# Performance work log

Measured on AMD Instinct MI355X. Metric: run time of the kernel, lower is better.

Reference implementation:

```python
import jax, jax.numpy as jnp
import numpy as np

N = 8192          # total neurons (n)
IN_NEURONS = 1024 # input_neurons
OUT_NEURONS = 256 # output_neurons


def setup_inputs() -> dict:
    key = jax.random.key(0)
    k1, k2 = jax.random.split(key)
    x = jax.random.normal(k1, (1, IN_NEURONS), dtype=jnp.float32)
    # learned adjacency weight (original uses kaiming_uniform; scale kept small for stability)
    W = jax.random.normal(k2, (N, N), dtype=jnp.float32) * 0.01
    return {"x": x, "W": W, "num_steps": 4}


def reference(x, W, num_steps):
    n = W.shape[0]
    # load_input_neurons: state = (W.T * pad(x[0], n)).T  ==  W * s0[:, None]
    s0 = jnp.pad(x[0], (0, n - x.shape[1]))        # [n]
    state = W * s0[:, None]                        # [n, n]

    # step(): next = sum_i(W.T * state[i]) then .T  ==  W * colsum(state)[:, None]
    def body(state, _):
        col_sum = state.sum(axis=0)                # [n]
        return W * col_sum[:, None], None

    state, _ = jax.lax.scan(body, state, None, length=num_steps)

    # extract_output_neurons: diagonal entries state[-i, -i], i = OUT..1
    return jnp.diagonal(state)[-OUT_NEURONS:]      # [OUT_NEURONS]
```

## Files before the change

kernel.cpp:

```cpp
#include <hip/hip_runtime.h>


namespace {
constexpr int N = 8192;
constexpr int NF4 = N / 4;
constexpr int IN_N = 1024;
constexpr int OUT_N = 256;
constexpr int BT = 256;

constexpr int B1 = 256;
constexpr int R1R = IN_N / B1;
constexpr int B2 = 1024;
constexpr int R2R = N / B2;

constexpr size_t OFF_V1 = 0;
constexpr size_t OFF_V2 = 8192;
constexpr size_t OFF_V3 = 16384;
constexpr size_t OFF_V4 = 24576;
constexpr size_t OFF_P  = 32768;

typedef float f4 __attribute__((ext_vector_type(4)));
}

__global__ void zero_vecs(float* __restrict__ ws) {
  int i = blockIdx.x * blockDim.x + threadIdx.x;
  if (i < 3 * N + OUT_N) ws[i] = 0.0f;
}

template <int ROWS>
__global__ __launch_bounds__(BT) void gemv_slab(const float* __restrict__ W,
                                                const float* __restrict__ vin,
                                                float* __restrict__ P) {
  __shared__ float sv[ROWS];
  const int b = blockIdx.x, t = threadIdx.x;
  const int i0 = b * ROWS;
  if (t < ROWS) sv[t] = vin[i0 + t];
  __syncthreads();
  const f4* __restrict__ W4 = reinterpret_cast<const f4*>(W);
  f4 acc[8];
#pragma unroll
  for (int k = 0; k < 8; ++k) acc[k] = (f4)(0.f);
#pragma unroll 2
  for (int i = 0; i < ROWS; ++i) {
    const float s = sv[i];
    const f4* __restrict__ row = W4 + (size_t)(i0 + i) * NF4;
#pragma unroll
    for (int k = 0; k < 8; ++k) {
      const f4 w = __builtin_nontemporal_load(row + k * BT + t);
      acc[k] += w * s;
    }
  }
  f4* __restrict__ P4 = reinterpret_cast<f4*>(P) + (size_t)b * NF4;
#pragma unroll
  for (int k = 0; k < 8; ++k) P4[k * BT + t] = acc[k];
}

template <int CS>
__global__ __launch_bounds__(BT) void reduce_cols(const float* __restrict__ P,
                                                  float* __restrict__ v) {
  const int j = blockIdx.x * BT + threadIdx.x;
  const int c0 = blockIdx.y * CS;
  float a = 0.f;
#pragma unroll 8
  for (int c = 0; c < CS; ++c) a += P[(size_t)(c0 + c) * N + j];
  atomicAdd(v + j, a);
}

__global__ __launch_bounds__(64) void gemv_tail(const float* __restrict__ W,
                                                const float* __restrict__ v3,
                                                float* __restrict__ v4) {
  __shared__ float sv[32];
  const int b = blockIdx.x, t = threadIdx.x;
  const int i0 = b * 32;
  if (t < 32) sv[t] = v3[i0 + t];
  __syncthreads();
  const f4* __restrict__ W4 = reinterpret_cast<const f4*>(W);
  f4 a = (f4)(0.f);
#pragma unroll 4
  for (int i = 0; i < 32; ++i) {
    const f4 w = W4[(size_t)(i0 + i) * NF4 + 1984 + t];
    a += w * sv[i];
  }
  atomicAdd(v4 + 4 * t + 0, a.x);
  atomicAdd(v4 + 4 * t + 1, a.y);
  atomicAdd(v4 + 4 * t + 2, a.z);
  atomicAdd(v4 + 4 * t + 3, a.w);
}

__global__ void diag_scale(const float* __restrict__ W,
                           const float* __restrict__ v4,
                           float* __restrict__ out) {
  const int t = threadIdx.x;
  const size_t j = (size_t)(N - OUT_N + t);
  out[t] = W[j * (N + 1)] * v4[t];
}

extern "C" void kernel_launch(void* const* d_in, const int* in_sizes, int n_in,
                              void* d_out, int out_size, void* d_ws, size_t ws_size,
                              hipStream_t stream) {
  const float* x = (const float*)d_in[0];
  const float* W = (const float*)d_in[1];
  float* ws = (float*)d_ws;
  float* v1 = ws + OFF_V1;
  float* v2 = ws + OFF_V2;
  float* v3 = ws + OFF_V3;
  float* v4 = ws + OFF_V4;
  float* P  = ws + OFF_P;
  float* out = (float*)d_out;

  zero_vecs<<<(3 * N + OUT_N + 255) / 256, 256, 0, stream>>>(ws);

  gemv_slab<R1R><<<B1, BT, 0, stream>>>(W, x, P);
  reduce_cols<32><<<dim3(N / BT, B1 / 32), BT, 0, stream>>>(P, v1);

  gemv_slab<R2R><<<B2, BT, 0, stream>>>(W, v1, P);
  reduce_cols<32><<<dim3(N / BT, B2 / 32), BT, 0, stream>>>(P, v2);

  gemv_slab<R2R><<<B2, BT, 0, stream>>>(W, v2, P);
  reduce_cols<32><<<dim3(N / BT, B2 / 32), BT, 0, stream>>>(P, v3);

  gemv_tail<<<N / 32, 64, 0, stream>>>(W, v3, v4);

  diag_scale<<<1, OUT_N, 0, stream>>>(W, v4, out);
}
```

Baseline: 445.2 us.

## Fuse column reduction into GEMV via atomics and prefetch next row

Removes the partial-sum buffer P and the separate reduce_cols kernels. Each GEMV block now atomically adds its per-column partial sums straight into the output vector. The row loop is fully unrolled with software prefetch of the next W row, and the first-stage block count is doubled. This cuts the write and re-read of the large partial buffer plus three launches, in exchange for many more global float atomics per column (1024 blocks × 8192 columns) and possible contention.

```diff
diff --git a/kernel.cpp b/kernel.cpp
--- a/kernel.cpp
+++ b/kernel.cpp
@@ -8,7 +8,7 @@
 constexpr int OUT_N = 256;
 constexpr int BT = 256;
 
-constexpr int B1 = 256;
+constexpr int B1 = 512;
 constexpr int R1R = IN_N / B1;
 constexpr int B2 = 1024;
 constexpr int R2R = N / B2;
@@ -17,53 +17,60 @@
 constexpr size_t OFF_V2 = 8192;
 constexpr size_t OFF_V3 = 16384;
 constexpr size_t OFF_V4 = 24576;
-constexpr size_t OFF_P  = 32768;
+constexpr int ZN = 3 * N + OUT_N;
 
 typedef float f4 __attribute__((ext_vector_type(4)));
 }
 
 __global__ void zero_vecs(float* __restrict__ ws) {
   int i = blockIdx.x * blockDim.x + threadIdx.x;
-  if (i < 3 * N + OUT_N) ws[i] = 0.0f;
+  if (i < ZN) ws[i] = 0.0f;
 }
 
 template <int ROWS>
-__global__ __launch_bounds__(BT) void gemv_slab(const float* __restrict__ W,
-                                                const float* __restrict__ vin,
-                                                float* __restrict__ P) {
+__global__ __launch_bounds__(BT) void gemv_slab_at(const float* __restrict__ W,
+                                                   const float* __restrict__ vin,
+                                                   float* __restrict__ vout) {
   __shared__ float sv[ROWS];
   const int b = blockIdx.x, t = threadIdx.x;
   const int i0 = b * ROWS;
   if (t < ROWS) sv[t] = vin[i0 + t];
   __syncthreads();
-  const f4* __restrict__ W4 = reinterpret_cast<const f4*>(W);
-  f4 acc[8];
+  const f4* __restrict__ W4 = reinterpret_cast<const f4*>(W) + (size_t)i0 * NF4;
+
+  f4 acc[8], cur[8];
 #pragma unroll
   for (int k = 0; k < 8; ++k) acc[k] = (f4)(0.f);
-#pragma unroll 2
-  for (int i = 0; i < ROWS; ++i) {
+#pragma unroll
+  for (int k = 0; k < 8; ++k)
+    cur[k] = __builtin_nontemporal_load(W4 + k * BT + t);
+
+#pragma unroll
+  for (int i = 0; i < ROWS - 1; ++i) {
+    f4 nxt[8];
+    const f4* __restrict__ row = W4 + (size_t)(i + 1) * NF4;
+#pragma unroll
+    for (int k = 0; k < 8; ++k)
+      nxt[k] = __builtin_nontemporal_load(row + k * BT + t);
     const float s = sv[i];
-    const f4* __restrict__ row = W4 + (size_t)(i0 + i) * NF4;
 #pragma unroll
-    for (int k = 0; k < 8; ++k) {
-      const f4 w = __builtin_nontemporal_load(row + k * BT + t);
-      acc[k] += w * s;
-    }
+    for (int k = 0; k < 8; ++k) acc[k] += cur[k] * s;
+#pragma unroll
+    for (int k = 0; k < 8; ++k) cur[k] = nxt[k];
   }
-  f4* __restrict__ P4 = reinterpret_cast<f4*>(P) + (size_t)b * NF4;
+  {
+    const float s = sv[ROWS - 1];
 #pragma unroll
-  for (int k = 0; k < 8; ++k) P4[k * BT + t] = acc[k];
-}
-
-template <int CS>
-__global__ __launch_bounds__(BT) void reduce_cols(const float* __restrict__ P,
-                                                  float* __restrict__ v) {
-  const int j = blockIdx.x * BT + threadIdx.x;
-  const int c0 = blockIdx.y * CS;
-  float a = 0.f;
-#pragma unroll 8
-  for (int c = 0; c < CS; ++c) a += P[(size_t)(c0 + c) * N + j];
-  atomicAdd(v + j, a);
+    for (int k = 0; k < 8; ++k) acc[k] += cur[k] * s;
+  }
+#pragma unroll
+  for (int k = 0; k < 8; ++k) {
+    const int j = (k * BT + t) * 4;
+    atomicAdd(vout + j + 0, acc[k].x);
+    atomicAdd(vout + j + 1, acc[k].y);
+    atomicAdd(vout + j + 2, acc[k].z);
+    atomicAdd(vout + j + 3, acc[k].w);
+  }
 }
 
 __global__ __launch_bounds__(64) void gemv_tail(const float* __restrict__ W,
@@ -78,7 +85,7 @@
   f4 a = (f4)(0.f);
 #pragma unroll 4
   for (int i = 0; i < 32; ++i) {
-    const f4 w = W4[(size_t)(i0 + i) * NF4 + 1984 + t];
+    const f4 w = __builtin_nontemporal_load(W4 + (size_t)(i0 + i) * NF4 + 1984 + t);
     a += w * sv[i];
   }
   atomicAdd(v4 + 4 * t + 0, a.x);
@@ -105,21 +112,12 @@
   float* v2 = ws + OFF_V2;
   float* v3 = ws + OFF_V3;
   float* v4 = ws + OFF_V4;
-  float* P  = ws + OFF_P;
   float* out = (float*)d_out;
 
-  zero_vecs<<<(3 * N + OUT_N + 255) / 256, 256, 0, stream>>>(ws);
-
-  gemv_slab<R1R><<<B1, BT, 0, stream>>>(W, x, P);
-  reduce_cols<32><<<dim3(N / BT, B1 / 32), BT, 0, stream>>>(P, v1);
-
-  gemv_slab<R2R><<<B2, BT, 0, stream>>>(W, v1, P);
-  reduce_cols<32><<<dim3(N / BT, B2 / 32), BT, 0, stream>>>(P, v2);
-
-  gemv_slab<R2R><<<B2, BT, 0, stream>>>(W, v2, P);
-  reduce_cols<32><<<dim3(N / BT, B2 / 32), BT, 0, stream>>>(P, v3);
-
+  zero_vecs<<<(ZN + 255) / 256, 256, 0, stream>>>(ws);
+  gemv_slab_at<R1R><<<B1, BT, 0, stream>>>(W, x, v1);
+  gemv_slab_at<R2R><<<B2, BT, 0, stream>>>(W, v1, v2);
+  gemv_slab_at<R2R><<<B2, BT, 0, stream>>>(W, v2, v3);
   gemv_tail<<<N / 32, 64, 0, stream>>>(W, v3, v4);
-
   diag_scale<<<1, OUT_N, 0, stream>>>(W, v4, out);
 }
```

New measurement: 729.9 us. +63.9%, slower.
